# Kernel tuning notes

Hardware: AMD Instinct MI355X
Metric: run time of the kernel (lower is better)

The kernel has to match this reference:

```python
import jax, jax.numpy as jnp
import numpy as np

N = 8192        # num nodes, > sparse_attention_threshold=5000 -> sparse attention path
IN = 128        # in_channels
OUT = 128       # out_channels
HEADS = 2       # attention_heads
DEG = 32        # avg degree used to build theta sparsity


def _xavier(key, shape):
    a = np.sqrt(6.0 / (shape[0] + shape[1])).astype(np.float32)
    return jax.random.uniform(key, shape, jnp.float32, -a, a)


def setup_inputs() -> dict:
    rng = np.random.default_rng(0)
    rows = np.repeat(np.arange(N), DEG)
    cols = rng.integers(0, N, size=N * DEG)
    theta_np = np.zeros((N, N), dtype=np.float32)
    theta_np[rows, cols] = 1.0
    # matches torch: rows, cols = np.where(theta > 1e-5)
    r, c = np.nonzero(theta_np > 1e-5)
    edge_index = jnp.asarray(np.stack([r, c]).astype(np.int32))  # [2, E]
    key = jax.random.key(0)
    ks = jax.random.split(key, 4)
    x = jax.random.normal(ks[0], (N, IN), jnp.float32)
    weight = _xavier(ks[1], (IN, OUT * HEADS))
    bias = jnp.zeros((OUT * HEADS,), jnp.float32)
    att_weight1 = _xavier(ks[2], (2 * OUT, OUT // 2))
    att_weight2 = _xavier(ks[3], (OUT // 2, 1))
    return {"x": x, "theta": jnp.asarray(theta_np), "weight": weight,
            "bias": bias, "att_weight1": att_weight1,
            "att_weight2": att_weight2, "edge_index": edge_index}


def _forward(x, weight, bias, att_weight1, att_weight2, edge_index):
    # x @ W + b, reshape to [N, heads, out]
    h = (x @ weight + bias).reshape(N, HEADS, OUT)
    src, dst = edge_index[0], edge_index[1]
    # cat([h_src, h_dst]) @ W1 == h_src @ W1[:OUT] + h_dst @ W1[OUT:]
    # project at node level first (cheaper), then gather per edge
    p_src = jnp.einsum('nhd,df->nhf', h, att_weight1[:OUT])
    p_dst = jnp.einsum('nhd,df->nhf', h, att_weight1[OUT:])
    s = jax.nn.leaky_relu(p_src[src] + p_dst[dst])               # [E, H, OUT//2]
    scores = jnp.einsum('ehf,fo->eho', s, att_weight2)[..., 0]    # [E, H]
    # torch does F.softmax(att_scores, dim=0): GLOBAL softmax over all edges per head
    att = jax.nn.softmax(scores, axis=0)                          # [E, H]
    # sparse COO mm: out[src] += att * h[dst]
    msgs = att[:, :, None] * h[dst]                               # [E, H, OUT]
    agg = jnp.zeros((N, HEADS, OUT), h.dtype).at[src].add(msgs)
    return agg.mean(axis=1)                                       # mean over heads -> [N, OUT]


def reference(x, theta, weight, bias, att_weight1, att_weight2, edge_index):
    # theta only determines the edge list (computed on CPU/numpy in the torch
    # code); edge_index is precomputed consistently in setup_inputs.
    del theta
    return _forward(x, weight, bias, att_weight1, att_weight2, edge_index)
```

## Files before the change

kernel.cpp:

```cpp
#include <hip/hip_runtime.h>
#include <hip/hip_bf16.h>

#define NN 8192
#define INC 128
#define HC 256
#define NPB 16
#define NGRP (NN / NPB)
#define SCORE_BLOCKS 1024

__global__ __launch_bounds__(256) void k_h_p(
    const float* __restrict__ x, const float* __restrict__ W,
    const float* __restrict__ bias, const float* __restrict__ att1,
    float* __restrict__ h, float* __restrict__ ps, float* __restrict__ pd,
    float* __restrict__ sums) {
  int t = threadIdx.x;
  int n0 = blockIdx.x * NPB;
  if (blockIdx.x == 0 && t < 2) sums[t] = 0.f;
  __shared__ float xs[NPB * INC];
  __shared__ float hs[NPB * HC];
  {
    const float4* xin = (const float4*)(x + (size_t)n0 * INC);
    ((float4*)xs)[t] = xin[t];
    ((float4*)xs)[t + 256] = xin[t + 256];
  }
  __syncthreads();
  {
    float acc[NPB];
    float b = bias[t];
    #pragma unroll
    for (int n = 0; n < NPB; ++n) acc[n] = b;
    #pragma unroll 2
    for (int d = 0; d < INC; ++d) {
      float w = W[d * HC + t];
      #pragma unroll
      for (int n = 0; n < NPB; ++n) acc[n] += xs[n * INC + d] * w;
    }
    #pragma unroll
    for (int n = 0; n < NPB; ++n) {
      h[((size_t)(n0 + n)) * HC + t] = acc[n];
      hs[n * HC + t] = acc[n];
    }
  }
  __syncthreads();
  int f = t & 63, sel = t >> 6;
  int hh = sel & 1, isdst = sel >> 1;
  const float* a1 = att1 + (isdst ? 128 * 64 : 0) + f;
  float p[NPB];
  #pragma unroll
  for (int n = 0; n < NPB; ++n) p[n] = 0.f;
  #pragma unroll 2
  for (int d = 0; d < 128; ++d) {
    float w = a1[d * 64];
    #pragma unroll
    for (int n = 0; n < NPB; ++n) p[n] += hs[n * HC + hh * 128 + d] * w;
  }
  float* dp = isdst ? pd : ps;
  #pragma unroll
  for (int n = 0; n < NPB; ++n)
    dp[((size_t)(n0 + n)) * 128 + hh * 64 + f] = p[n];
}

__global__ __launch_bounds__(256) void k_score(
    const float* __restrict__ ps, const float* __restrict__ pd,
    const int* __restrict__ ei, const float* __restrict__ att2,
    float* __restrict__ exps, float* __restrict__ sums,
    int* __restrict__ offs, int E) {
  __shared__ float w2[64];
  __shared__ float ssum[2];
  int t = threadIdx.x;
  if (t < 64) w2[t] = att2[t];
  if (t < 2) ssum[t] = 0.f;
  __syncthreads();
  int g = t >> 4, sub = t & 15;
  int total = E * 2;
  float runsum = 0.f;
  for (int pair = blockIdx.x * 16 + g; pair < total; pair += SCORE_BLOCKS * 16) {
    int hh = pair & 1;
    int e = pair >> 1;
    int s = ei[e], dt = ei[E + e];
    float4 av = *(const float4*)&ps[((size_t)s * 2 + hh) * 64 + sub * 4];
    float4 bv = *(const float4*)&pd[((size_t)dt * 2 + hh) * 64 + sub * 4];
    float vx = av.x + bv.x; vx = vx > 0.f ? vx : 0.01f * vx;
    float vy = av.y + bv.y; vy = vy > 0.f ? vy : 0.01f * vy;
    float vz = av.z + bv.z; vz = vz > 0.f ? vz : 0.01f * vz;
    float vw = av.w + bv.w; vw = vw > 0.f ? vw : 0.01f * vw;
    float sc = vx * w2[sub * 4] + vy * w2[sub * 4 + 1] + vz * w2[sub * 4 + 2] + vw * w2[sub * 4 + 3];
    #pragma unroll
    for (int off = 8; off; off >>= 1) sc += __shfl_down(sc, off, 16);
    if (sub == 0) {
      float ev = __expf(sc);
      exps[pair] = ev;
      runsum += ev;
      if (hh == 0) {
        if (e == 0) offs[0] = 0;
        else if (ei[e] != ei[e - 1]) offs[ei[e]] = e;
        if (e == E - 1) offs[NN] = E;
      }
    }
  }
  runsum += __shfl_xor(runsum, 32);
  int lane = t & 63;
  if (lane == 0 || lane == 16) atomicAdd(&ssum[(t >> 4) & 1], runsum);
  __syncthreads();
  if (t < 2) atomicAdd(&sums[t], ssum[t]);
}

__global__ __launch_bounds__(256) void k_agg(
    const float* __restrict__ h, const float* __restrict__ exps,
    const float* __restrict__ sums, const int* __restrict__ ei,
    const int* __restrict__ offs, float* __restrict__ out, int E) {
  int n = blockIdx.x, t = threadIdx.x;
  int lo = offs[n], hi = offs[n + 1];
  int hh = t >> 7;
  float inv = 1.0f / sums[hh];
  float acc = 0.f;
  int e = lo;
  for (; e + 4 <= hi; e += 4) {
    int d0 = ei[E + e], d1 = ei[E + e + 1], d2 = ei[E + e + 2], d3 = ei[E + e + 3];
    float w0 = exps[2 * e + hh],        w1 = exps[2 * (e + 1) + hh];
    float w2v = exps[2 * (e + 2) + hh], w3 = exps[2 * (e + 3) + hh];
    float h0 = h[(size_t)d0 * HC + t], h1 = h[(size_t)d1 * HC + t];
    float h2 = h[(size_t)d2 * HC + t], h3 = h[(size_t)d3 * HC + t];
    acc += w0 * h0 + w1 * h1 + w2v * h2 + w3 * h3;
  }
  for (; e < hi; ++e)
    acc += exps[2 * e + hh] * h[(size_t)ei[E + e] * HC + t];
  acc *= inv;
  __shared__ float l[HC];
  l[t] = acc;
  __syncthreads();
  if (t < 128)
    out[(size_t)n * 128 + t] = 0.5f * (l[t] + l[128 + t]);
}

extern "C" void kernel_launch(void* const* d_in, const int* in_sizes, int n_in,
                              void* d_out, int out_size, void* d_ws, size_t ws_size,
                              hipStream_t stream) {
  const float* x    = (const float*)d_in[0];
  const float* W    = (const float*)d_in[2];
  const float* bias = (const float*)d_in[3];
  const float* att1 = (const float*)d_in[4];
  const float* att2 = (const float*)d_in[5];
  const int* ei = (const int*)d_in[6];
  int E = in_sizes[6] / 2;
  float* out = (float*)d_out;

  float* ws = (float*)d_ws;
  float* h      = ws;
  float* ps     = h  + (size_t)NN * HC;
  float* pd     = ps + (size_t)NN * 128;
  float* exps   = pd + (size_t)NN * 128;
  float* sums   = exps + (size_t)E * 2;
  int*   offs   = (int*)(sums + 2);

  k_h_p<<<NGRP, 256, 0, stream>>>(x, W, bias, att1, h, ps, pd, sums);
  k_score<<<SCORE_BLOCKS, 256, 0, stream>>>(ps, pd, ei, att2, exps, sums, offs, E);
  k_agg<<<NN, 256, 0, stream>>>(h, exps, sums, ei, offs, out, E);
}
```

Baseline: 431.5 us.

## Fuse edge scoring into per-node aggregation and defer global softmax normalization

```diff
diff --git a/kernel.cpp b/kernel.cpp
--- a/kernel.cpp
+++ b/kernel.cpp
@@ -6,16 +6,21 @@
 #define HC 256
 #define NPB 16
 #define NGRP (NN / NPB)
-#define SCORE_BLOCKS 1024
+#define SCALE_BLOCKS 512
 
 __global__ __launch_bounds__(256) void k_h_p(
     const float* __restrict__ x, const float* __restrict__ W,
     const float* __restrict__ bias, const float* __restrict__ att1,
-    float* __restrict__ h, float* __restrict__ ps, float* __restrict__ pd,
-    float* __restrict__ sums) {
+    const int* __restrict__ ei, float* __restrict__ h,
+    float* __restrict__ ps, float* __restrict__ pd,
+    int* __restrict__ offs, int E) {
   int t = threadIdx.x;
   int n0 = blockIdx.x * NPB;
-  if (blockIdx.x == 0 && t < 2) sums[t] = 0.f;
+  for (int e = blockIdx.x * 256 + t; e < E; e += NGRP * 256) {
+    if (e == 0) offs[0] = 0;
+    else { int s1 = ei[e]; if (s1 != ei[e - 1]) offs[s1] = e; }
+    if (e == E - 1) offs[NN] = E;
+  }
   __shared__ float xs[NPB * INC];
   __shared__ float hs[NPB * HC];
   {
@@ -60,77 +65,83 @@
     dp[((size_t)(n0 + n)) * 128 + hh * 64 + f] = p[n];
 }
 
-__global__ __launch_bounds__(256) void k_score(
-    const float* __restrict__ ps, const float* __restrict__ pd,
-    const int* __restrict__ ei, const float* __restrict__ att2,
-    float* __restrict__ exps, float* __restrict__ sums,
-    int* __restrict__ offs, int E) {
-  __shared__ float w2[64];
-  __shared__ float ssum[2];
-  int t = threadIdx.x;
-  if (t < 64) w2[t] = att2[t];
-  if (t < 2) ssum[t] = 0.f;
+__global__ __launch_bounds__(256) void k_agg(
+    const float* __restrict__ h, const float* __restrict__ ps,
+    const float* __restrict__ pd, const int* __restrict__ ei,
+    const float* __restrict__ att2, const int* __restrict__ offs,
+    float* __restrict__ raw, float* __restrict__ part, int E) {
+  int n = blockIdx.x, t = threadIdx.x;
+  __shared__ float psl[128];
+  __shared__ float w2l[64];
+  __shared__ float red[4 * HC];
+  __shared__ float rs[4][2];
+  if (t < 128) psl[t] = ps[(size_t)n * 128 + t];
+  if (t < 64) w2l[t] = att2[t];
   __syncthreads();
-  int g = t >> 4, sub = t & 15;
-  int total = E * 2;
-  float runsum = 0.f;
-  for (int pair = blockIdx.x * 16 + g; pair < total; pair += SCORE_BLOCKS * 16) {
-    int hh = pair & 1;
-    int e = pair >> 1;
-    int s = ei[e], dt = ei[E + e];
-    float4 av = *(const float4*)&ps[((size_t)s * 2 + hh) * 64 + sub * 4];
-    float4 bv = *(const float4*)&pd[((size_t)dt * 2 + hh) * 64 + sub * 4];
-    float vx = av.x + bv.x; vx = vx > 0.f ? vx : 0.01f * vx;
-    float vy = av.y + bv.y; vy = vy > 0.f ? vy : 0.01f * vy;
-    float vz = av.z + bv.z; vz = vz > 0.f ? vz : 0.01f * vz;
-    float vw = av.w + bv.w; vw = vw > 0.f ? vw : 0.01f * vw;
-    float sc = vx * w2[sub * 4] + vy * w2[sub * 4 + 1] + vz * w2[sub * 4 + 2] + vw * w2[sub * 4 + 3];
-    #pragma unroll
-    for (int off = 8; off; off >>= 1) sc += __shfl_down(sc, off, 16);
-    if (sub == 0) {
-      float ev = __expf(sc);
-      exps[pair] = ev;
-      runsum += ev;
-      if (hh == 0) {
-        if (e == 0) offs[0] = 0;
-        else if (ei[e] != ei[e - 1]) offs[ei[e]] = e;
-        if (e == E - 1) offs[NN] = E;
-      }
-    }
+  int wid = t >> 6, lane = t & 63;
+  int head = lane >> 5, j = lane & 31;
+  int lo = offs[n], hi = offs[n + 1];
+  float pa = psl[head * 64 + j * 2], pb = psl[head * 64 + j * 2 + 1];
+  float wa = w2l[j * 2], wb = w2l[j * 2 + 1];
+  float4 acc = {0.f, 0.f, 0.f, 0.f};
+  float rsum = 0.f;
+  for (int e = lo + wid; e < hi; e += 4) {
+    int dst = ei[E + e];
+    float4 h4 = *(const float4*)&h[(size_t)dst * HC + lane * 4];
+    float2 pdv = *(const float2*)&pd[(size_t)dst * 128 + head * 64 + j * 2];
+    float v0 = pa + pdv.x; v0 = v0 > 0.f ? v0 : 0.01f * v0;
+    float v1 = pb + pdv.y; v1 = v1 > 0.f ? v1 : 0.01f * v1;
+    float sc = v0 * wa + v1 * wb;
+    sc += __shfl_xor(sc, 1);  sc += __shfl_xor(sc, 2);  sc += __shfl_xor(sc, 4);
+    sc += __shfl_xor(sc, 8);  sc += __shfl_xor(sc, 16);
+    float ev = __expf(sc);
+    if (j == 0) rsum += ev;
+    acc.x += ev * h4.x; acc.y += ev * h4.y; acc.z += ev * h4.z; acc.w += ev * h4.w;
   }
-  runsum += __shfl_xor(runsum, 32);
-  int lane = t & 63;
-  if (lane == 0 || lane == 16) atomicAdd(&ssum[(t >> 4) & 1], runsum);
+  ((float4*)red)[wid * 64 + lane] = acc;
+  if (j == 0) rs[wid][head] = rsum;
   __syncthreads();
-  if (t < 2) atomicAdd(&sums[t], ssum[t]);
+  float tot = red[t] + red[HC + t] + red[2 * HC + t] + red[3 * HC + t];
+  raw[(size_t)n * HC + t] = tot;
+  if (t < 2)
+    part[n * 2 + t] = rs[0][t] + rs[1][t] + rs[2][t] + rs[3][t];
 }
 
-__global__ __launch_bounds__(256) void k_agg(
-    const float* __restrict__ h, const float* __restrict__ exps,
-    const float* __restrict__ sums, const int* __restrict__ ei,
-    const int* __restrict__ offs, float* __restrict__ out, int E) {
-  int n = blockIdx.x, t = threadIdx.x;
-  int lo = offs[n], hi = offs[n + 1];
-  int hh = t >> 7;
-  float inv = 1.0f / sums[hh];
-  float acc = 0.f;
-  int e = lo;
-  for (; e + 4 <= hi; e += 4) {
-    int d0 = ei[E + e], d1 = ei[E + e + 1], d2 = ei[E + e + 2], d3 = ei[E + e + 3];
-    float w0 = exps[2 * e + hh],        w1 = exps[2 * (e + 1) + hh];
-    float w2v = exps[2 * (e + 2) + hh], w3 = exps[2 * (e + 3) + hh];
-    float h0 = h[(size_t)d0 * HC + t], h1 = h[(size_t)d1 * HC + t];
-    float h2 = h[(size_t)d2 * HC + t], h3 = h[(size_t)d3 * HC + t];
-    acc += w0 * h0 + w1 * h1 + w2v * h2 + w3 * h3;
+__global__ __launch_bounds__(256) void k_scale(
+    const float* __restrict__ raw, const float* __restrict__ part,
+    float* __restrict__ out) {
+  int t = threadIdx.x;
+  float s0 = 0.f, s1 = 0.f;
+  #pragma unroll 4
+  for (int k = 0; k < 32; ++k) {
+    float2 p = ((const float2*)part)[t + 256 * k];
+    s0 += p.x; s1 += p.y;
   }
-  for (; e < hi; ++e)
-    acc += exps[2 * e + hh] * h[(size_t)ei[E + e] * HC + t];
-  acc *= inv;
-  __shared__ float l[HC];
-  l[t] = acc;
+  #pragma unroll
+  for (int off = 1; off <= 32; off <<= 1) {
+    s0 += __shfl_xor(s0, off);
+    s1 += __shfl_xor(s1, off);
+  }
+  __shared__ float ws0[4], ws1[4];
+  if ((t & 63) == 0) { ws0[t >> 6] = s0; ws1[t >> 6] = s1; }
   __syncthreads();
-  if (t < 128)
-    out[(size_t)n * 128 + t] = 0.5f * (l[t] + l[128 + t]);
+  float inv0 = 1.f / (ws0[0] + ws0[1] + ws0[2] + ws0[3]);
+  float inv1 = 1.f / (ws1[0] + ws1[1] + ws1[2] + ws1[3]);
+  const float4* r4 = (const float4*)raw;
+  float4* o4 = (float4*)out;
+  int idx = blockIdx.x * 256 + t;
+  #pragma unroll
+  for (int rep = 0; rep < 2; ++rep, idx += SCALE_BLOCKS * 256) {
+    int nn = idx >> 5, c4 = idx & 31;
+    float4 a = r4[nn * 64 + c4];
+    float4 b = r4[nn * 64 + 32 + c4];
+    float4 o;
+    o.x = 0.5f * (a.x * inv0 + b.x * inv1);
+    o.y = 0.5f * (a.y * inv0 + b.y * inv1);
+    o.z = 0.5f * (a.z * inv0 + b.z * inv1);
+    o.w = 0.5f * (a.w * inv0 + b.w * inv1);
+    o4[idx] = o;
+  }
 }
 
 extern "C" void kernel_launch(void* const* d_in, const int* in_sizes, int n_in,
@@ -146,14 +157,14 @@
   float* out = (float*)d_out;
 
   float* ws = (float*)d_ws;
-  float* h      = ws;
-  float* ps     = h  + (size_t)NN * HC;
-  float* pd     = ps + (size_t)NN * 128;
-  float* exps   = pd + (size_t)NN * 128;
-  float* sums   = exps + (size_t)E * 2;
-  int*   offs   = (int*)(sums + 2);
+  float* h    = ws;
+  float* ps   = h  + (size_t)NN * HC;
+  float* pd   = ps + (size_t)NN * 128;
+  float* raw  = pd + (size_t)NN * 128;
+  float* part = raw + (size_t)NN * HC;
+  int*   offs = (int*)(part + (size_t)NN * 2);
 
-  k_h_p<<<NGRP, 256, 0, stream>>>(x, W, bias, att1, h, ps, pd, sums);
-  k_score<<<SCORE_BLOCKS, 256, 0, stream>>>(ps, pd, ei, att2, exps, sums, offs, E);
-  k_agg<<<NN, 256, 0, stream>>>(h, exps, sums, ei, offs, out, E);
+  k_h_p<<<NGRP, 256, 0, stream>>>(x, W, bias, att1, ei, h, ps, pd, offs, E);
+  k_agg<<<NN, 256, 0, stream>>>(h, ps, pd, ei, att2, offs, raw, part, E);
+  k_scale<<<SCALE_BLOCKS, 256, 0, stream>>>(raw, part, out);
 }
```

Result: faster. 406.8 us (-5.7%).
